# Performance work log

Hardware: AMD Instinct MI355X
Metric: run time of the kernel (lower is better)

Reference implementation:

```python
import jax, jax.numpy as jnp
import numpy as np

N_IN, M_MID = 512, 256
B, H, W = 16, 64, 64

def setup_inputs() -> dict:
    key = jax.random.key(0)
    ks = jax.random.split(key, 7)
    s = 0.05
    return {
        "x": jax.random.normal(ks[0], (B, N_IN, H, W), dtype=jnp.float32),
        "W_state": jax.random.normal(ks[1], (M_MID, N_IN), dtype=jnp.float32) * s,
        "b_state": jax.random.normal(ks[2], (M_MID,), dtype=jnp.float32) * s,
        "W_proj": jax.random.normal(ks[3], (M_MID, N_IN), dtype=jnp.float32) * s,
        "b_proj": jax.random.normal(ks[4], (M_MID,), dtype=jnp.float32) * s,
        "W_extend": jax.random.normal(ks[5], (N_IN, M_MID), dtype=jnp.float32) * s,
        "b_extend": jax.random.normal(ks[6], (N_IN,), dtype=jnp.float32) * s,
    }

def reference(x, W_state, b_state, W_proj, b_proj, W_extend, b_extend):
    n, c, h, w = x.shape
    hw = h * w
    xf = x.reshape(n, c, hw)                                   # [n, C, HW]
    # 1x1 convs are channel GEMMs over flattened spatial dim
    x_state = jnp.einsum('mc,nch->nmh', W_state, xf) + b_state[None, :, None]   # [n, M, HW]
    x_proj = jnp.einsum('mc,nch->nmh', W_proj, xf) + b_proj[None, :, None]      # [n, M, HW]
    # bmm -> scale -> softmax -> bmm (graph reasoning over M x M)
    scores = jnp.einsum('nmh,nkh->nmk', x_state, x_proj) / jnp.sqrt(jnp.float32(hw))
    attn = jax.nn.softmax(scores, axis=2)                      # [n, M, M]
    x_rstate = jnp.einsum('nmk,nkh->nmh', attn, x_proj)        # [n, M, HW]
    # extend back to C channels + residual
    ext = jnp.einsum('cm,nmh->nch', W_extend, x_rstate) + b_extend[None, :, None]
    return x + ext.reshape(n, c, h, w)
```

## Files before the change

kernel.cpp:

```cpp
#include <hip/hip_runtime.h>
#include <hip/hip_bf16.h>
#include <stdint.h>

typedef __bf16 bf16x8_t __attribute__((ext_vector_type(8)));
typedef float  f32x4_t  __attribute__((ext_vector_type(4)));
typedef short  short8_t __attribute__((ext_vector_type(8)));

__device__ __forceinline__ unsigned short f2b(float f) {
    union { float f; unsigned u; } v; v.f = f;
    unsigned u = v.u;
    return (unsigned short)((u + 0x7FFFu + ((u >> 16) & 1u)) >> 16);
}

#define AS3(p) ((__attribute__((address_space(3))) void*)(p))
#define AS1(p) ((const __attribute__((address_space(1))) void*)(p))

#define NB   16
#define CIN  512
#define MMID 256
#define HW   4096
#define KSPLIT 8

__global__ __launch_bounds__(256) void prep_weights(
    const float* __restrict__ Ws, const float* __restrict__ Wp,
    const float* __restrict__ Wef, const float* __restrict__ bs,
    const float* __restrict__ bp,
    unsigned short* __restrict__ Wsp, unsigned short* __restrict__ Wex,
    float* __restrict__ bsp)
{
    int i = blockIdx.x * 256 + threadIdx.x;
    if (i < MMID * CIN) {
        Wsp[i]              = f2b(Ws[i]);
        Wsp[MMID * CIN + i] = f2b(Wp[i]);
        Wex[i]              = f2b(Wef[i]);
    }
    if (i < MMID) { bsp[i] = bs[i]; bsp[MMID + i] = bp[i]; }
}

__global__ __launch_bounds__(256) void transpose_convert_x(
    const float* __restrict__ x, unsigned short* __restrict__ xT)
{
    __shared__ unsigned short tile[64][66];
    const int n = blockIdx.z, c0 = blockIdx.y * 64, h0 = blockIdx.x * 64;
    const float* s = x + ((size_t)n * CIN + c0) * HW + h0;
    unsigned short* d = xT + ((size_t)n * HW + h0) * CIN + c0;
    const int t = threadIdx.x;
    {
        const int rr = t >> 4, cc = (t & 15) * 4;
        #pragma unroll
        for (int p = 0; p < 4; ++p) {
            int r = p * 16 + rr;
            float4 v = *(const float4*)(s + (size_t)r * HW + cc);
            tile[r][cc + 0] = f2b(v.x); tile[r][cc + 1] = f2b(v.y);
            tile[r][cc + 2] = f2b(v.z); tile[r][cc + 3] = f2b(v.w);
        }
    }
    __syncthreads();
    {
        const int wr = t >> 3, wc = (t & 7) * 8;
        #pragma unroll
        for (int p = 0; p < 2; ++p) {
            int h = p * 32 + wr;
            unsigned short tmp[8];
            #pragma unroll
            for (int j = 0; j < 8; ++j) tmp[j] = tile[wc + j][h];
            *(short8_t*)(d + (size_t)h * CIN + wc) = *(const short8_t*)tmp;
        }
    }
}

__global__ __launch_bounds__(256) void transpose_bf16_64(
    const unsigned short* __restrict__ src, unsigned short* __restrict__ dst,
    int srs, int drs, long long sbs, long long dbs)
{
    __shared__ unsigned short tile[64][66];
    const int n = blockIdx.z, r0 = blockIdx.y * 64, c0 = blockIdx.x * 64;
    const unsigned short* s = src + (size_t)n * sbs + (size_t)r0 * srs + c0;
    unsigned short* d = dst + (size_t)n * dbs + (size_t)c0 * drs + r0;
    const int t = threadIdx.x;
    const int rr = t >> 3, cc = (t & 7) * 8;
    #pragma unroll
    for (int p = 0; p < 2; ++p) {
        int r = p * 32 + rr;
        short8_t v = *(const short8_t*)(s + (size_t)r * srs + cc);
        #pragma unroll
        for (int j = 0; j < 8; ++j) tile[r][cc + j] = ((const unsigned short*)&v)[j];
    }
    __syncthreads();
    #pragma unroll
    for (int p = 0; p < 2; ++p) {
        int c = p * 32 + rr;
        unsigned short tmp[8];
        #pragma unroll
        for (int j = 0; j < 8; ++j) tmp[j] = tile[cc + j][c];
        *(short8_t*)(d + (size_t)c * drs + cc) = *(const short8_t*)tmp;
    }
}

template <int EPI>
__device__ __forceinline__ void epilogue_repack(
    f32x4_t (&acc)[4][4], unsigned short* smem,
    int m0, int n0, int wave, int lane,
    const float* __restrict__ bias, const float* __restrict__ resid,
    void* __restrict__ Cout, int ldc, size_t cbase)
{
    float* fbuf = (float*)smem;
    const int t   = wave * 64 + lane;
    const int l15 = lane & 15, l16 = lane >> 4;
    const int wr2 = wave >> 1;
    const int wc  = (wave & 1) * 64;

    #pragma unroll
    for (int p = 0; p < 4; ++p) {
        __syncthreads();
        if (wr2 == (p >> 1)) {
            const int ihalf = p & 1;
            #pragma unroll
            for (int i2 = 0; i2 < 2; ++i2) {
                const int i = ihalf * 2 + i2;
                #pragma unroll
                for (int r = 0; r < 4; ++r) {
                    const int lrow = i2 * 16 + l16 * 4 + r;
                    #pragma unroll
                    for (int j = 0; j < 4; ++j)
                        fbuf[lrow * 132 + wc + j * 16 + l15] = acc[i][j][r];
                }
            }
        }
        __syncthreads();
        #pragma unroll
        for (int it = 0; it < 2; ++it) {
            const int lrow = it * 16 + (t >> 4);
            const int col  = (t & 15) * 8;
            const int row  = m0 + p * 32 + lrow;
            float v[8];
            *(float4*)&v[0] = *(const float4*)&fbuf[lrow * 132 + col];
            *(float4*)&v[4] = *(const float4*)&fbuf[lrow * 132 + col + 4];
            float badd = 0.f;
            if constexpr (EPI == 0 || EPI == 3) badd = bias[row];
            const size_t idx = cbase + (size_t)row * ldc + n0 + col;
            if constexpr (EPI == 3) {
                float o[8];
                const float* rp = resid + idx;
                float4 r0 = *(const float4*)rp;
                float4 r1 = *(const float4*)(rp + 4);
                o[0] = v[0] + badd + r0.x; o[1] = v[1] + badd + r0.y;
                o[2] = v[2] + badd + r0.z; o[3] = v[3] + badd + r0.w;
                o[4] = v[4] + badd + r1.x; o[5] = v[5] + badd + r1.y;
                o[6] = v[6] + badd + r1.z; o[7] = v[7] + badd + r1.w;
                float* op = (float*)Cout + idx;
                *(float4*)op = *(const float4*)&o[0];
                *(float4*)(op + 4) = *(const float4*)&o[4];
            } else if constexpr (EPI == 1) {
                float* op = (float*)Cout + idx;
                *(float4*)op = *(const float4*)&v[0];
                *(float4*)(op + 4) = *(const float4*)&v[4];
            } else {
                unsigned short o[8];
                #pragma unroll
                for (int k = 0; k < 8; ++k) o[k] = f2b(v[k] + badd);
                *(short8_t*)((unsigned short*)Cout + idx) = *(const short8_t*)o;
            }
        }
    }
}

__global__ __launch_bounds__(256) void gemm_scores(
    const unsigned short* __restrict__ Ysp, float* __restrict__ scoresP)
{
    __shared__ unsigned short smem[2 * 128 * 64];
    unsigned short* As = smem;
    unsigned short* Bs = smem + 128 * 64;

    const int z  = blockIdx.z;
    const int n  = z >> 3;
    const int kc = z & 7;
    const int m0 = blockIdx.y * 128;
    const int n0 = blockIdx.x * 128;

    const unsigned short* Ab = Ysp + (size_t)n * CIN * HW + (size_t)m0 * HW;
    const unsigned short* Bb = Ysp + (size_t)n * CIN * HW + (size_t)(MMID + n0) * HW;

    const int t    = threadIdx.x;
    const int lane = t & 63;
    const int wave = t >> 6;
    const int wr   = (wave >> 1) * 64;
    const int wc   = (wave & 1) * 64;
    const int l15  = lane & 15;
    const int l16  = lane >> 4;

    f32x4_t acc[4][4] = {};

    const int kbeg = kc * (HW / KSPLIT);
    for (int k0 = kbeg; k0 < kbeg + HW / KSPLIT; k0 += 64) {
        #pragma unroll
        for (int c = 0; c < 4; ++c) {
            const int o   = (c * 256 + t) * 16;
            const int row = o >> 7;
            const int ce  = (o & 127) >> 1;
            __builtin_amdgcn_global_load_lds(
                AS1(Ab + (size_t)row * HW + k0 + ce), AS3((char*)As + o), 16, 0, 0);
            __builtin_amdgcn_global_load_lds(
                AS1(Bb + (size_t)row * HW + k0 + ce), AS3((char*)Bs + o), 16, 0, 0);
        }
        asm volatile("s_waitcnt vmcnt(0)" ::: "memory");
        __syncthreads();

        #pragma unroll
        for (int ks = 0; ks < 2; ++ks) {
            bf16x8_t af[4], bfr[4];
            const int kb = ks * 32 + l16 * 8;
            #pragma unroll
            for (int i = 0; i < 4; ++i) {
                af[i]  = *(const bf16x8_t*)(As + (wr + i * 16 + l15) * 64 + kb);
                bfr[i] = *(const bf16x8_t*)(Bs + (wc + i * 16 + l15) * 64 + kb);
            }
            #pragma unroll
            for (int i = 0; i < 4; ++i)
                #pragma unroll
                for (int j = 0; j < 4; ++j)
                    acc[i][j] = __builtin_amdgcn_mfma_f32_16x16x32_bf16(af[i], bfr[j], acc[i][j], 0, 0, 0);
        }
        __syncthreads();
    }

    float* outp = scoresP + (size_t)(kc * NB + n) * MMID * MMID;
    epilogue_repack<1>(acc, smem, m0, n0, wave, lane, nullptr, nullptr,
                       outp, MMID, 0);
}

__global__ __launch_bounds__(64) void softmax_rows(
    const float* __restrict__ scoresP, unsigned short* __restrict__ attn)
{
    const size_t row = blockIdx.x;
    const int l = threadIdx.x;
    const size_t pstride = (size_t)NB * MMID * MMID;
    float4 v = {0.f, 0.f, 0.f, 0.f};
    #pragma unroll
    for (int p = 0; p < KSPLIT; ++p) {
        float4 u = *(const float4*)(scoresP + p * pstride + row * MMID + l * 4);
        v.x += u.x; v.y += u.y; v.z += u.z; v.w += u.w;
    }
    float mx = fmaxf(fmaxf(v.x, v.y), fmaxf(v.z, v.w));
    #pragma unroll
    for (int off = 32; off; off >>= 1) mx = fmaxf(mx, __shfl_xor(mx, off));
    const float sc = 0.015625f;
    float e0 = __expf((v.x - mx) * sc), e1 = __expf((v.y - mx) * sc);
    float e2 = __expf((v.z - mx) * sc), e3 = __expf((v.w - mx) * sc);
    float sum = e0 + e1 + e2 + e3;
    #pragma unroll
    for (int off = 32; off; off >>= 1) sum += __shfl_xor(sum, off);
    const float inv = 1.0f / sum;
    unsigned short o[4] = { f2b(e0 * inv), f2b(e1 * inv), f2b(e2 * inv), f2b(e3 * inv) };
    *(uint64_t*)(attn + row * MMID + l * 4) = *(const uint64_t*)o;
}

template <int EPI>
__global__ __launch_bounds__(256) void gemm_nt(
    const unsigned short* __restrict__ A, const unsigned short* __restrict__ B,
    int lda, int ldb, int K,
    long long strideA, long long strideB,
    const float* __restrict__ bias,
    const float* __restrict__ resid,
    void* __restrict__ Cout, int ldc, long long strideC)
{
    __shared__ unsigned short smem[2 * 128 * 64];
    unsigned short* As = smem;
    unsigned short* Bs = smem + 128 * 64;

    const int n  = blockIdx.z;
    const int m0 = blockIdx.y * 128;
    const int n0 = blockIdx.x * 128;

    const unsigned short* Ab = A + (size_t)n * strideA + (size_t)m0 * lda;
    const unsigned short* Bb = B + (size_t)n * strideB + (size_t)n0 * ldb;

    const int t    = threadIdx.x;
    const int lane = t & 63;
    const int wave = t >> 6;
    const int wr   = (wave >> 1) * 64;
    const int wc   = (wave & 1) * 64;
    const int l15  = lane & 15;
    const int l16  = lane >> 4;

    f32x4_t acc[4][4] = {};

    for (int k0 = 0; k0 < K; k0 += 64) {
        #pragma unroll
        for (int c = 0; c < 4; ++c) {
            const int o   = (c * 256 + t) * 16;
            const int row = o >> 7;
            const int ce  = (o & 127) >> 1;
            __builtin_amdgcn_global_load_lds(
                AS1(Ab + (size_t)row * lda + k0 + ce), AS3((char*)As + o), 16, 0, 0);
            __builtin_amdgcn_global_load_lds(
                AS1(Bb + (size_t)row * ldb + k0 + ce), AS3((char*)Bs + o), 16, 0, 0);
        }
        asm volatile("s_waitcnt vmcnt(0)" ::: "memory");
        __syncthreads();

        #pragma unroll
        for (int ks = 0; ks < 2; ++ks) {
            bf16x8_t af[4], bfr[4];
            const int kb = ks * 32 + l16 * 8;
            #pragma unroll
            for (int i = 0; i < 4; ++i) {
                af[i]  = *(const bf16x8_t*)(As + (wr + i * 16 + l15) * 64 + kb);
                bfr[i] = *(const bf16x8_t*)(Bs + (wc + i * 16 + l15) * 64 + kb);
            }
            #pragma unroll
            for (int i = 0; i < 4; ++i)
                #pragma unroll
                for (int j = 0; j < 4; ++j)
                    acc[i][j] = __builtin_amdgcn_mfma_f32_16x16x32_bf16(af[i], bfr[j], acc[i][j], 0, 0, 0);
        }
        __syncthreads();
    }

    epilogue_repack<EPI>(acc, smem, m0, n0, wave, lane, bias, resid,
                         Cout, ldc, (size_t)n * strideC);
}

extern "C" void kernel_launch(void* const* d_in, const int* in_sizes, int n_in,
                              void* d_out, int out_size, void* d_ws, size_t ws_size,
                              hipStream_t stream)
{
    const float* x   = (const float*)d_in[0];
    const float* Ws  = (const float*)d_in[1];
    const float* bs  = (const float*)d_in[2];
    const float* Wp  = (const float*)d_in[3];
    const float* bp  = (const float*)d_in[4];
    const float* Wef = (const float*)d_in[5];
    const float* be  = (const float*)d_in[6];
    float* out = (float*)d_out;

    unsigned short* xT     = (unsigned short*)d_ws;
    unsigned short* Ysp    = xT     + (size_t)NB * HW * CIN;
    unsigned short* xprojT = Ysp    + (size_t)NB * CIN * HW;
    unsigned short* Wsp    = xprojT + (size_t)NB * HW * MMID;
    unsigned short* Wex    = Wsp    + (size_t)CIN * CIN;
    unsigned short* attn   = Wex    + (size_t)CIN * MMID;
    unsigned short* attnT  = attn   + (size_t)NB * MMID * MMID;
    unsigned short* G      = attnT  + (size_t)NB * MMID * MMID;
    float* bsp = (float*)(G + (size_t)NB * CIN * MMID);
    float* scoresP = (float*)xT;

    prep_weights<<<512, 256, 0, stream>>>(Ws, Wp, Wef, bs, bp, Wsp, Wex, bsp);

    transpose_convert_x<<<dim3(HW / 64, CIN / 64, NB), 256, 0, stream>>>(x, xT);

    gemm_nt<0><<<dim3(HW / 128, CIN / 128, NB), 256, 0, stream>>>(
        Wsp, xT, CIN, CIN, CIN, 0LL, (long long)HW * CIN,
        bsp, nullptr, Ysp, HW, (long long)CIN * HW);

    transpose_bf16_64<<<dim3(HW / 64, MMID / 64, NB), 256, 0, stream>>>(
        Ysp + (size_t)MMID * HW, xprojT, HW, MMID,
        (long long)CIN * HW, (long long)HW * MMID);

    gemm_scores<<<dim3(MMID / 128, MMID / 128, NB * KSPLIT), 256, 0, stream>>>(Ysp, scoresP);

    softmax_rows<<<NB * MMID, 64, 0, stream>>>(scoresP, attn);

    transpose_bf16_64<<<dim3(MMID / 64, MMID / 64, NB), 256, 0, stream>>>(
        attn, attnT, MMID, MMID, (long long)MMID * MMID, (long long)MMID * MMID);

    gemm_nt<2><<<dim3(MMID / 128, CIN / 128, NB), 256, 0, stream>>>(
        Wex, attnT, MMID, MMID, MMID,
        0LL, (long long)MMID * MMID,
        nullptr, nullptr, G, MMID, (long long)CIN * MMID);

    gemm_nt<3><<<dim3(HW / 128, CIN / 128, NB), 256, 0, stream>>>(
        G, xprojT, MMID, MMID, MMID,
        (long long)CIN * MMID, (long long)HW * MMID,
        be, x, out, HW, (long long)CIN * HW);
}
```

Measured before the change: 227.5 us.

## Double-buffer GEMM K-loop, swizzle block order, fuse xproj transpose into conv GEMM

Replaces the single-buffered K-loop in every GEMM with a shared double-buffered macro that prefetches the next K tile into LDS while computing the current one. Launches all GEMMs on a flat 1D grid with an XCD-aware swizzle that remaps block IDs. The conv GEMM gets a custom epilogue that also writes the transposed projection directly, removing the separate transpose kernel. These cut global-load latency stalls, improve L2 locality and drop one launch plus a round trip through memory. The cost is doubled LDS use per block, which may lower occupancy.

```diff
diff --git a/kernel.cpp b/kernel.cpp
--- a/kernel.cpp
+++ b/kernel.cpp
@@ -20,6 +20,16 @@
 #define MMID 256
 #define HW   4096
 #define KSPLIT 8
+#define ASZ  (128 * 64)
+
+__device__ __forceinline__ void swz3(int gx, int gy, int& bx, int& by, int& bz) {
+    const int nwg = gridDim.x, ord = blockIdx.x, q = nwg >> 3;
+    const int s = (ord & 7) * q + (ord >> 3);
+    bx = s % gx;
+    const int rem = s / gx;
+    by = rem % gy;
+    bz = rem / gy;
+}
 
 __global__ __launch_bounds__(256) void prep_weights(
     const float* __restrict__ Ws, const float* __restrict__ Wp,
@@ -165,21 +175,62 @@
     }
 }
 
-__global__ __launch_bounds__(256) void gemm_scores(
-    const unsigned short* __restrict__ Ysp, float* __restrict__ scoresP)
-{
-    __shared__ unsigned short smem[2 * 128 * 64];
-    unsigned short* As = smem;
-    unsigned short* Bs = smem + 128 * 64;
-
-    const int z  = blockIdx.z;
-    const int n  = z >> 3;
-    const int kc = z & 7;
-    const int m0 = blockIdx.y * 128;
-    const int n0 = blockIdx.x * 128;
-
-    const unsigned short* Ab = Ysp + (size_t)n * CIN * HW + (size_t)m0 * HW;
-    const unsigned short* Bb = Ysp + (size_t)n * CIN * HW + (size_t)(MMID + n0) * HW;
+#define GEMM_KLOOP(Ab, Bb, lda, ldb, KBEG, NT)                                          \
+    auto stage = [&](int k0, int b) {                                                   \
+        unsigned short* Asb = smem + b * 2 * ASZ;                                       \
+        unsigned short* Bsb = Asb + ASZ;                                                \
+        _Pragma("unroll")                                                               \
+        for (int c = 0; c < 4; ++c) {                                                   \
+            const int o   = (c * 256 + t) * 16;                                         \
+            const int row = o >> 7;                                                     \
+            const int ce  = (o & 127) >> 1;                                             \
+            __builtin_amdgcn_global_load_lds(                                           \
+                AS1(Ab + (size_t)row * lda + k0 + ce), AS3((char*)Asb + o), 16, 0, 0);  \
+            __builtin_amdgcn_global_load_lds(                                           \
+                AS1(Bb + (size_t)row * ldb + k0 + ce), AS3((char*)Bsb + o), 16, 0, 0);  \
+        }                                                                               \
+    };                                                                                  \
+    stage(KBEG, 0);                                                                     \
+    asm volatile("s_waitcnt vmcnt(0)" ::: "memory");                                    \
+    __syncthreads();                                                                    \
+    for (int itk = 0; itk < (NT); ++itk) {                                              \
+        const int cur = itk & 1;                                                        \
+        if (itk + 1 < (NT)) stage(KBEG + (itk + 1) * 64, cur ^ 1);                      \
+        const unsigned short* Asb = smem + cur * 2 * ASZ;                               \
+        const unsigned short* Bsb = Asb + ASZ;                                          \
+        _Pragma("unroll")                                                               \
+        for (int ks = 0; ks < 2; ++ks) {                                                \
+            bf16x8_t af[4], bfr[4];                                                     \
+            const int kb = ks * 32 + l16 * 8;                                           \
+            _Pragma("unroll")                                                           \
+            for (int i = 0; i < 4; ++i) {                                               \
+                af[i]  = *(const bf16x8_t*)(Asb + (wr + i * 16 + l15) * 64 + kb);       \
+                bfr[i] = *(const bf16x8_t*)(Bsb + (wc + i * 16 + l15) * 64 + kb);       \
+            }                                                                           \
+            _Pragma("unroll")                                                           \
+            for (int i = 0; i < 4; ++i)                                                 \
+                _Pragma("unroll")                                                       \
+                for (int j = 0; j < 4; ++j)                                             \
+                    acc[i][j] = __builtin_amdgcn_mfma_f32_16x16x32_bf16(                \
+                        af[i], bfr[j], acc[i][j], 0, 0, 0);                             \
+        }                                                                               \
+        asm volatile("s_waitcnt vmcnt(0)" ::: "memory");                                \
+        __syncthreads();                                                                \
+    }
+
+__global__ __launch_bounds__(256) void gemm_conv(
+    const unsigned short* __restrict__ Wsp, const unsigned short* __restrict__ xT,
+    const float* __restrict__ bsp,
+    unsigned short* __restrict__ Ysp, unsigned short* __restrict__ xprojT)
+{
+    __shared__ unsigned short smem[4 * ASZ];
+
+    int bx, by, n;  swz3(HW / 128, CIN / 128, bx, by, n);
+    const int m0 = by * 128;
+    const int h0 = bx * 128;
+
+    const unsigned short* Ab = Wsp + (size_t)m0 * CIN;
+    const unsigned short* Bb = xT + (size_t)n * HW * CIN + (size_t)h0 * CIN;
 
     const int t    = threadIdx.x;
     const int lane = t & 63;
@@ -190,39 +241,84 @@
     const int l16  = lane >> 4;
 
     f32x4_t acc[4][4] = {};
-
+    GEMM_KLOOP(Ab, Bb, CIN, CIN, 0, CIN / 64)
+
+    float* fbuf = (float*)smem;
+    const int wr2 = wave >> 1;
+    unsigned short* Yb = Ysp + (size_t)n * CIN * HW;
+    #pragma unroll
+    for (int p = 0; p < 4; ++p) {
+        __syncthreads();
+        if (wr2 == (p >> 1)) {
+            const int ihalf = p & 1;
+            #pragma unroll
+            for (int i2 = 0; i2 < 2; ++i2) {
+                const int i = ihalf * 2 + i2;
+                #pragma unroll
+                for (int r = 0; r < 4; ++r) {
+                    const int lrow = i2 * 16 + l16 * 4 + r;
+                    #pragma unroll
+                    for (int j = 0; j < 4; ++j)
+                        fbuf[lrow * 132 + wc + j * 16 + l15] = acc[i][j][r];
+                }
+            }
+        }
+        __syncthreads();
+        #pragma unroll
+        for (int it = 0; it < 2; ++it) {
+            const int lrow = it * 16 + (t >> 4);
+            const int col  = (t & 15) * 8;
+            const int row  = m0 + p * 32 + lrow;
+            const float badd = bsp[row];
+            float v[8];
+            *(float4*)&v[0] = *(const float4*)&fbuf[lrow * 132 + col];
+            *(float4*)&v[4] = *(const float4*)&fbuf[lrow * 132 + col + 4];
+            unsigned short o8[8];
+            #pragma unroll
+            for (int k = 0; k < 8; ++k) o8[k] = f2b(v[k] + badd);
+            *(short8_t*)(Yb + (size_t)row * HW + h0 + col) = *(const short8_t*)o8;
+        }
+        if (m0 >= MMID) {
+            const int h = t >> 1, ksub = (t & 1) * 16;
+            unsigned short o16[16];
+            #pragma unroll
+            for (int i = 0; i < 16; ++i) {
+                const int lr = ksub + i;
+                o16[i] = f2b(fbuf[lr * 132 + h] + bsp[m0 + p * 32 + lr]);
+            }
+            unsigned short* dp = xprojT + ((size_t)n * HW + h0 + h) * MMID
+                                 + (m0 - MMID) + p * 32 + ksub;
+            *(short8_t*)dp       = *(const short8_t*)&o16[0];
+            *(short8_t*)(dp + 8) = *(const short8_t*)&o16[8];
+        }
+    }
+}
+
+__global__ __launch_bounds__(256) void gemm_scores(
+    const unsigned short* __restrict__ Ysp, float* __restrict__ scoresP)
+{
+    __shared__ unsigned short smem[4 * ASZ];
+
+    int bx, by, z;  swz3(MMID / 128, MMID / 128, bx, by, z);
+    const int n  = z >> 3;
+    const int kc = z & 7;
+    const int m0 = by * 128;
+    const int n0 = bx * 128;
+
+    const unsigned short* Ab = Ysp + (size_t)n * CIN * HW + (size_t)m0 * HW;
+    const unsigned short* Bb = Ysp + (size_t)n * CIN * HW + (size_t)(MMID + n0) * HW;
+
+    const int t    = threadIdx.x;
+    const int lane = t & 63;
+    const int wave = t >> 6;
+    const int wr   = (wave >> 1) * 64;
+    const int wc   = (wave & 1) * 64;
+    const int l15  = lane & 15;
+    const int l16  = lane >> 4;
+
+    f32x4_t acc[4][4] = {};
     const int kbeg = kc * (HW / KSPLIT);
-    for (int k0 = kbeg; k0 < kbeg + HW / KSPLIT; k0 += 64) {
-        #pragma unroll
-        for (int c = 0; c < 4; ++c) {
-            const int o   = (c * 256 + t) * 16;
-            const int row = o >> 7;
-            const int ce  = (o & 127) >> 1;
-            __builtin_amdgcn_global_load_lds(
-                AS1(Ab + (size_t)row * HW + k0 + ce), AS3((char*)As + o), 16, 0, 0);
-            __builtin_amdgcn_global_load_lds(
-                AS1(Bb + (size_t)row * HW + k0 + ce), AS3((char*)Bs + o), 16, 0, 0);
-        }
-        asm volatile("s_waitcnt vmcnt(0)" ::: "memory");
-        __syncthreads();
-
-        #pragma unroll
-        for (int ks = 0; ks < 2; ++ks) {
-            bf16x8_t af[4], bfr[4];
-            const int kb = ks * 32 + l16 * 8;
-            #pragma unroll
-            for (int i = 0; i < 4; ++i) {
-                af[i]  = *(const bf16x8_t*)(As + (wr + i * 16 + l15) * 64 + kb);
-                bfr[i] = *(const bf16x8_t*)(Bs + (wc + i * 16 + l15) * 64 + kb);
-            }
-            #pragma unroll
-            for (int i = 0; i < 4; ++i)
-                #pragma unroll
-                for (int j = 0; j < 4; ++j)
-                    acc[i][j] = __builtin_amdgcn_mfma_f32_16x16x32_bf16(af[i], bfr[j], acc[i][j], 0, 0, 0);
-        }
-        __syncthreads();
-    }
+    GEMM_KLOOP(Ab, Bb, HW, HW, kbeg, (HW / KSPLIT) / 64)
 
     float* outp = scoresP + (size_t)(kc * NB + n) * MMID * MMID;
     epilogue_repack<1>(acc, smem, m0, n0, wave, lane, nullptr, nullptr,
@@ -262,15 +358,14 @@
     long long strideA, long long strideB,
     const float* __restrict__ bias,
     const float* __restrict__ resid,
-    void* __restrict__ Cout, int ldc, long long strideC)
-{
-    __shared__ unsigned short smem[2 * 128 * 64];
-    unsigned short* As = smem;
-    unsigned short* Bs = smem + 128 * 64;
-
-    const int n  = blockIdx.z;
-    const int m0 = blockIdx.y * 128;
-    const int n0 = blockIdx.x * 128;
+    void* __restrict__ Cout, int ldc, long long strideC,
+    int gx, int gy)
+{
+    __shared__ unsigned short smem[4 * ASZ];
+
+    int bx, by, n;  swz3(gx, gy, bx, by, n);
+    const int m0 = by * 128;
+    const int n0 = bx * 128;
 
     const unsigned short* Ab = A + (size_t)n * strideA + (size_t)m0 * lda;
     const unsigned short* Bb = B + (size_t)n * strideB + (size_t)n0 * ldb;
@@ -284,38 +379,7 @@
     const int l16  = lane >> 4;
 
     f32x4_t acc[4][4] = {};
-
-    for (int k0 = 0; k0 < K; k0 += 64) {
-        #pragma unroll
-        for (int c = 0; c < 4; ++c) {
-            const int o   = (c * 256 + t) * 16;
-            const int row = o >> 7;
-            const int ce  = (o & 127) >> 1;
-            __builtin_amdgcn_global_load_lds(
-                AS1(Ab + (size_t)row * lda + k0 + ce), AS3((char*)As + o), 16, 0, 0);
-            __builtin_amdgcn_global_load_lds(
-                AS1(Bb + (size_t)row * ldb + k0 + ce), AS3((char*)Bs + o), 16, 0, 0);
-        }
-        asm volatile("s_waitcnt vmcnt(0)" ::: "memory");
-        __syncthreads();
-
-        #pragma unroll
-        for (int ks = 0; ks < 2; ++ks) {
-            bf16x8_t af[4], bfr[4];
-            const int kb = ks * 32 + l16 * 8;
-            #pragma unroll
-            for (int i = 0; i < 4; ++i) {
-                af[i]  = *(const bf16x8_t*)(As + (wr + i * 16 + l15) * 64 + kb);
-                bfr[i] = *(const bf16x8_t*)(Bs + (wc + i * 16 + l15) * 64 + kb);
-            }
-            #pragma unroll
-            for (int i = 0; i < 4; ++i)
-                #pragma unroll
-                for (int j = 0; j < 4; ++j)
-                    acc[i][j] = __builtin_amdgcn_mfma_f32_16x16x32_bf16(af[i], bfr[j], acc[i][j], 0, 0, 0);
-        }
-        __syncthreads();
-    }
+    GEMM_KLOOP(Ab, Bb, lda, ldb, 0, K / 64)
 
     epilogue_repack<EPI>(acc, smem, m0, n0, wave, lane, bias, resid,
                          Cout, ldc, (size_t)n * strideC);
@@ -349,28 +413,26 @@
 
     transpose_convert_x<<<dim3(HW / 64, CIN / 64, NB), 256, 0, stream>>>(x, xT);
 
-    gemm_nt<0><<<dim3(HW / 128, CIN / 128, NB), 256, 0, stream>>>(
-        Wsp, xT, CIN, CIN, CIN, 0LL, (long long)HW * CIN,
-        bsp, nullptr, Ysp, HW, (long long)CIN * HW);
-
-    transpose_bf16_64<<<dim3(HW / 64, MMID / 64, NB), 256, 0, stream>>>(
-        Ysp + (size_t)MMID * HW, xprojT, HW, MMID,
-        (long long)CIN * HW, (long long)HW * MMID);
-
-    gemm_scores<<<dim3(MMID / 128, MMID / 128, NB * KSPLIT), 256, 0, stream>>>(Ysp, scoresP);
+    gemm_conv<<<(HW / 128) * (CIN / 128) * NB, 256, 0, stream>>>(
+        Wsp, xT, bsp, Ysp, xprojT);
+
+    gemm_scores<<<(MMID / 128) * (MMID / 128) * NB * KSPLIT, 256, 0, stream>>>(
+        Ysp, scoresP);
 
     softmax_rows<<<NB * MMID, 64, 0, stream>>>(scoresP, attn);
 
     transpose_bf16_64<<<dim3(MMID / 64, MMID / 64, NB), 256, 0, stream>>>(
         attn, attnT, MMID, MMID, (long long)MMID * MMID, (long long)MMID * MMID);
 
-    gemm_nt<2><<<dim3(MMID / 128, CIN / 128, NB), 256, 0, stream>>>(
+    gemm_nt<2><<<(MMID / 128) * (CIN / 128) * NB, 256, 0, stream>>>(
         Wex, attnT, MMID, MMID, MMID,
         0LL, (long long)MMID * MMID,
-        nullptr, nullptr, G, MMID, (long long)CIN * MMID);
-
-    gemm_nt<3><<<dim3(HW / 128, CIN / 128, NB), 256, 0, stream>>>(
+        nullptr, nullptr, G, MMID, (long long)CIN * MMID,
+        MMID / 128, CIN / 128);
+
+    gemm_nt<3><<<(HW / 128) * (CIN / 128) * NB, 256, 0, stream>>>(
         G, xprojT, MMID, MMID, MMID,
         (long long)CIN * MMID, (long long)HW * MMID,
-        be, x, out, HW, (long long)CIN * HW);
-}
+        be, x, out, HW, (long long)CIN * HW,
+        HW / 128, CIN / 128);
+}
```

After: 212.7 us. 1.07x faster.
